# Kernel optimization log

Measured on AMD Instinct MI355X. Metric: run time of the kernel, lower is better.

Reference implementation:

```python
import jax, jax.numpy as jnp
import numpy as np
from jax import lax

RENDER_SIZE = (228, 304)   # (H, W) from __init__ default
FAR = 100.0                # z-buffer init, matches depth_map fill in source
EPS = 1e-7
CHUNK = 128                # faces processed per scan step


def setup_inputs() -> dict:
    key = jax.random.key(0)
    k1, k2, k3 = jax.random.split(key, 3)
    B, N, M = 1, 8192, 2048
    H, W = RENDER_SIZE
    uv = jax.random.uniform(k1, (B, N, 2), dtype=jnp.float32)           # u,v in [0,1]
    d = jax.random.uniform(k2, (B, N, 1), dtype=jnp.float32) * 4.0 + 1.0  # depth in [1,5]
    verts = jnp.concatenate([uv, d], axis=-1)                            # [B,N,3] depthmap format
    faces = jax.random.randint(k3, (B, M, 3), 0, N)                      # [B,M,3]
    fx = fy = 260.0
    K = jnp.array([[fx, 0.0, W / 2.0], [0.0, fy, H / 2.0], [0.0, 0.0, 1.0]], jnp.float32)
    intrinsics = jnp.tile(K[None], (B, 1, 1))
    ang = 0.02  # small camera rotation about y
    R = jnp.array([[np.cos(ang), 0.0, np.sin(ang)], [0.0, 1.0, 0.0],
                   [-np.sin(ang), 0.0, np.cos(ang)]], jnp.float32)
    R_mat = jnp.tile(R[None], (B, 1, 1))
    t_mat = jnp.tile(jnp.array([[0.01], [0.0], [0.02]], jnp.float32)[None], (B, 1, 1))
    return {"verts": verts, "faces": faces, "intrinsics": intrinsics,
            "R_mat": R_mat, "t_mat": t_mat}


def _convert_depthmap_to_cam(verts, K, H, W):
    # depthmap (u,v,d) -> camera coords; mirrors convert_depthmap_to_cam
    d = verts[..., 2:3]
    pix = jnp.concatenate([verts[..., 0:1] * W, verts[..., 1:2] * H,
                           jnp.ones_like(d)], axis=-1)                   # [B,N,3]
    Kinv = jnp.linalg.inv(K)
    return jnp.einsum('bij,bnj->bni', Kinv, pix) * d


def _project_cam_to_depthmap(cam, K, H, W):
    # camera coords -> depthmap (u,v,z); mirrors project_cam_to_depthmap
    z = cam[..., 2]
    p = jnp.stack([cam[..., 0] / (z + EPS), cam[..., 1] / (z + EPS),
                   jnp.ones_like(z)], axis=-1)
    p = jnp.einsum('bnj,bij->bni', p, K)  # matmul(p, K^T)
    u = jnp.clip(p[..., 0] / W, 0.0, 1.0)
    v = jnp.clip(p[..., 1] / H, 0.0, 1.0)
    return jnp.stack([u, v, z], axis=-1)


def _transform_depthmap(verts, K, R, t, H, W):
    cam = _convert_depthmap_to_cam(verts, K, H, W)                       # [B,N,3]
    cam2 = jnp.einsum('bij,bnj->bni', R, cam) + t[:, :, 0][:, None, :]   # R@x + t
    return _project_cam_to_depthmap(cam2, K, H, W)


def _rasterize(face_verts, S):
    """face_verts: [B,M,3,3] NDC (x,y) + depth z. Returns depth [B,S,S], sil [B,S,S]."""
    B, M = face_verts.shape[0], face_verts.shape[1]
    p = (2.0 * jnp.arange(S, dtype=face_verts.dtype) + 1.0 - S) / S      # NR pixel centers
    XP = p[None, None, None, :]   # x varies along last axis
    YP = p[None, None, :, None]   # y varies along rows

    chunks = face_verts.reshape(B, M // CHUNK, CHUNK, 3, 3).transpose(1, 0, 2, 3, 4)

    def step(carry, fvc):  # fvc: [B,C,3,3]
        depth, sil = carry
        x = fvc[..., 0][..., None, None]  # [B,C,3,1,1]
        y = fvc[..., 1][..., None, None]
        z = fvc[..., 2][..., None, None]
        x0, x1, x2 = x[:, :, 0], x[:, :, 1], x[:, :, 2]
        y0, y1, y2 = y[:, :, 0], y[:, :, 1], y[:, :, 2]
        z0, z1, z2 = z[:, :, 0], z[:, :, 1], z[:, :, 2]
        denom = (y1 - y2) * (x0 - x2) + (x2 - x1) * (y0 - y2)
        ok = jnp.abs(denom) > 1e-10
        safe = jnp.where(ok, denom, 1.0)
        w0 = ((y1 - y2) * (XP - x2) + (x2 - x1) * (YP - y2)) / safe      # [B,C,S,S]
        w1 = ((y2 - y0) * (XP - x2) + (x0 - x2) * (YP - y2)) / safe
        w2 = 1.0 - w0 - w1
        inside = (w0 >= 0) & (w1 >= 0) & (w2 >= 0) & ok
        inv_z = w0 / z0 + w1 / z1 + w2 / z2  # perspective-correct depth interp
        zp = 1.0 / jnp.where(jnp.abs(inv_z) > EPS, inv_z, EPS)
        zc = jnp.where(inside & (zp > 0), zp, FAR)
        depth = jnp.minimum(depth, zc.min(axis=1))                       # z-buffer update
        sil = jnp.maximum(sil, inside.any(axis=1).astype(depth.dtype))
        return (depth, sil), None

    init = (jnp.full((B, S, S), FAR, face_verts.dtype),
            jnp.zeros((B, S, S), face_verts.dtype))
    (depth, sil), _ = lax.scan(step, init, chunks)
    return depth, sil


def reference(verts, faces, intrinsics, R_mat, t_mat):
    H, W = RENDER_SIZE
    S = max(H, W)
    v = _transform_depthmap(verts, intrinsics, R_mat, t_mat, H, W)       # reprojected depthmap
    # depthmap [0,1] -> NDC [-1,1], keeping aspect via img_max_size
    ndc = jnp.concatenate([v[:, :, :1] * W / S * 2.0 - 1.0,
                           v[:, :, 1:2] * H / S * 2.0 - 1.0,
                           v[:, :, 2:]], axis=2)
    fv = jax.vmap(lambda vb, fb: vb[fb])(ndc, faces)                     # [B,M,3,3]
    depth, sil = _rasterize(fv, S)
    depth = depth[:, ::-1, :][:, :H, :W]  # flip(dim=1) then crop, as in _render
    sil = sil[:, ::-1, :][:, :H, :W]
    return jnp.stack([depth, sil], axis=1)  # [B,2,H,W]: depth + silhouette
```

## Files before the change

kernel.cpp:

```cpp
#include <hip/hip_runtime.h>

#define SS 304
#define HH 228
#define WW 304
#define FARV 100.0f
#define EPSV 1e-07f
#define SPLIT 16
#define CH 128

__device__ __forceinline__ void xform_vertex(
    float u, float v, float d,
    float fx, float cx, float fy, float cy,
    float r00, float r01, float r02,
    float r10, float r11, float r12,
    float r20, float r21, float r22,
    float t0, float t1, float t2,
    float& xn, float& yn, float& z)
{
#pragma clang fp contract(off)
    float ki00 = 1.0f / fx;
    float ki02 = -(cx / fx);
    float ki11 = 1.0f / fy;
    float ki12 = -(cy / fy);
    float px = u * (float)WW;
    float py = v * (float)HH;
    float c0 = (ki00 * px + ki02) * d;
    float c1 = (ki11 * py + ki12) * d;
    float c2 = d;
    float e0 = ((r00*c0 + r01*c1) + r02*c2) + t0;
    float e1 = ((r10*c0 + r11*c1) + r12*c2) + t1;
    float e2 = ((r20*c0 + r21*c1) + r22*c2) + t2;
    z = e2;
    float zd = z + EPSV;
    float p0 = e0 / zd;
    float p1 = e1 / zd;
    float q0 = p0 * fx + cx;
    float q1 = p1 * fy + cy;
    float uu = q0 / (float)WW; uu = fminf(fmaxf(uu, 0.0f), 1.0f);
    float vv = q1 / (float)HH; vv = fminf(fmaxf(vv, 0.0f), 1.0f);
    xn = uu * (float)WW / (float)SS * 2.0f - 1.0f;
    yn = vv * (float)HH / (float)SS * 2.0f - 1.0f;
}

__global__ __launch_bounds__(256) void prep_kernel(
    const float* __restrict__ verts,
    const int* __restrict__ faces,
    const float* __restrict__ Km,
    const float* __restrict__ Rm,
    const float* __restrict__ tm,
    float4* __restrict__ bboxArr,
    float4* __restrict__ G0arr,
    float4* __restrict__ G1arr,
    float2* __restrict__ G2arr,
    float* __restrict__ out, int M)
{
#pragma clang fp contract(off)
    int g = blockIdx.x * blockDim.x + threadIdx.x;
    if (g < HH * WW) {
        out[g] = FARV;
        out[HH * WW + g] = 0.0f;
    }
    if (g >= M) return;
    int m = g;
    int i0 = faces[3*m+0], i1 = faces[3*m+1], i2 = faces[3*m+2];
    float fx = Km[0], cx = Km[2], fy = Km[4], cy = Km[5];
    float r00 = Rm[0], r01 = Rm[1], r02 = Rm[2];
    float r10 = Rm[3], r11 = Rm[4], r12 = Rm[5];
    float r20 = Rm[6], r21 = Rm[7], r22 = Rm[8];
    float t0 = tm[0], t1 = tm[1], t2 = tm[2];

    float x0, y0, z0, x1, y1, z1, x2, y2, z2;
    xform_vertex(verts[3*i0+0], verts[3*i0+1], verts[3*i0+2], fx,cx,fy,cy,
                 r00,r01,r02,r10,r11,r12,r20,r21,r22,t0,t1,t2, x0,y0,z0);
    xform_vertex(verts[3*i1+0], verts[3*i1+1], verts[3*i1+2], fx,cx,fy,cy,
                 r00,r01,r02,r10,r11,r12,r20,r21,r22,t0,t1,t2, x1,y1,z1);
    xform_vertex(verts[3*i2+0], verts[3*i2+1], verts[3*i2+2], fx,cx,fy,cy,
                 r00,r01,r02,r10,r11,r12,r20,r21,r22,t0,t1,t2, x2,y2,z2);

    float A0 = y1 - y2;
    float B0 = x2 - x1;
    float A1 = y2 - y0;
    float B1 = x0 - x2;
    float dy02 = y0 - y2;
    float denom = A0 * B1 + B0 * dy02;
    bool ok = fabsf(denom) > 1e-10f;

    float xmin, xmax, ymin, ymax;
    if (ok) {
        xmin = fminf(x0, fminf(x1, x2)) - 1e-4f;
        xmax = fmaxf(x0, fmaxf(x1, x2)) + 1e-4f;
        ymin = fminf(y0, fminf(y1, y2)) - 1e-4f;
        ymax = fmaxf(y0, fmaxf(y1, y2)) + 1e-4f;
    } else {
        xmin = 1e30f; xmax = -1e30f; ymin = 1e30f; ymax = -1e30f;
    }
    bboxArr[m] = make_float4(xmin, xmax, ymin, ymax);

    float flip = (denom >= 0.0f) ? 1.0f : -1.0f;
    float sabs = fabsf(denom);
    float A0p = flip * A0, B0p = flip * B0;
    float C0p = -(A0p * x2 + B0p * y2);
    float A1p = flip * A1, B1p = flip * B1;
    float C1p = -(A1p * x2 + B1p * y2);
    float rz0 = 1.0f / z0, rz1 = 1.0f / z1, rz2 = 1.0f / z2;
    float D0 = rz0 / sabs, D1 = rz1 / sabs, D2 = rz2 / sabs;
    float d02 = D0 - D2, d12 = D1 - D2;
    float E = A0p * d02 + A1p * d12;
    float F = B0p * d02 + B1p * d12;
    float G = (C0p * d02 + C1p * d12) + sabs * D2;

    G0arr[m] = make_float4(A0p, B0p, C0p, sabs);
    G1arr[m] = make_float4(A1p, B1p, C1p, G);
    G2arr[m] = make_float2(E, F);
}

__global__ __launch_bounds__(256) void raster_kernel(
    const float4* __restrict__ bboxArr,
    const float4* __restrict__ G0arr,
    const float4* __restrict__ G1arr,
    const float2* __restrict__ G2arr,
    float* __restrict__ out, int M)
{
    __shared__ float4 sG0[CH];
    __shared__ float4 sG1[CH];
    __shared__ float2 sG2[CH];
    __shared__ int sCount;

    int tx = threadIdx.x, ty = threadIdx.y;
    int tid = ty * 16 + tx;
    int w = blockIdx.x * 16 + tx;
    int h = blockIdx.y * 16 + ty;

    int wlo = blockIdx.x * 16;
    int whi = min(wlo + 15, WW - 1);
    int hlo = blockIdx.y * 16;
    int hhi = min(hlo + 15, HH - 1);
    float txlo = ((float)(2*wlo + 1 - SS)) / (float)SS;
    float txhi = ((float)(2*whi + 1 - SS)) / (float)SS;
    float tylo = ((float)(2*(SS-1-hhi) + 1 - SS)) / (float)SS;
    float tyhi = ((float)(2*(SS-1-hlo) + 1 - SS)) / (float)SS;

    if (tid == 0) sCount = 0;
    __syncthreads();

    if (tid < CH) {
        int m = blockIdx.z * CH + tid;
        float4 rb = bboxArr[m];
        bool pass = !(rb.x > txhi || rb.y < txlo || rb.z > tyhi || rb.w < tylo);
        if (pass) {
            int i = atomicAdd(&sCount, 1);
            sG0[i] = G0arr[m];
            sG1[i] = G1arr[m];
            sG2[i] = G2arr[m];
        }
    }
    __syncthreads();
    int cnt = sCount;

    if (h < HH) {
        int irow = SS - 1 - h;
        float XP = ((float)(2*w    + 1 - SS)) / (float)SS;
        float YP = ((float)(2*irow + 1 - SS)) / (float)SS;

        float mx = 0.0f;

        for (int k = 0; k < cnt; ++k) {
            float4 g0 = sG0[k];
            float4 g1 = sG1[k];
            float2 g2 = sG2[k];
            float n0 = fmaf(g0.x, XP, fmaf(g0.y, YP, g0.z));
            float n1 = fmaf(g1.x, XP, fmaf(g1.y, YP, g1.z));
            float n2 = (g0.w - n0) - n1;
            float iz = fmaf(g2.x, XP, fmaf(g2.y, YP, g1.w));
            float m3 = fminf(fminf(n0, n1), n2);
            float cand = (m3 >= 0.0f) ? iz : 0.0f;
            mx = fmaxf(mx, cand);
        }

        if (mx > 0.0f) {
            float depth = __builtin_amdgcn_rcpf(mx);
            atomicMin((unsigned int*)&out[h * WW + w], __float_as_uint(depth));
            atomicMax((unsigned int*)&out[HH * WW + h * WW + w],
                      __float_as_uint(1.0f));
        }
    }
}

extern "C" void kernel_launch(void* const* d_in, const int* in_sizes, int n_in,
                              void* d_out, int out_size, void* d_ws, size_t ws_size,
                              hipStream_t stream) {
    const float* verts = (const float*)d_in[0];
    const int*   faces = (const int*)d_in[1];
    const float* K     = (const float*)d_in[2];
    const float* R     = (const float*)d_in[3];
    const float* t     = (const float*)d_in[4];
    float* out = (float*)d_out;

    int M = in_sizes[1] / 3;

    char* ws = (char*)d_ws;
    float4* bbox = (float4*)ws;                ws += (size_t)M * sizeof(float4);
    float4* G0   = (float4*)ws;                ws += (size_t)M * sizeof(float4);
    float4* G1   = (float4*)ws;                ws += (size_t)M * sizeof(float4);
    float2* G2   = (float2*)ws;                ws += (size_t)M * sizeof(float2);

    prep_kernel<<<(HH * WW + 255) / 256, 256, 0, stream>>>(
        verts, faces, K, R, t, bbox, G0, G1, G2, out, M);

    dim3 blk(16, 16);
    dim3 grd((WW + 15) / 16, (HH + 15) / 16, SPLIT);
    raster_kernel<<<grd, blk, 0, stream>>>(bbox, G0, G1, G2, out, M);
}
```

Measured before the change: 90.21 us.

## Rasterize 2x4 pixels per thread with incremental edge functions on 32x32 tiles

```diff
diff --git a/kernel.cpp b/kernel.cpp
--- a/kernel.cpp
+++ b/kernel.cpp
@@ -7,6 +7,7 @@
 #define EPSV 1e-07f
 #define SPLIT 16
 #define CH 128
+#define TILE 32
 
 __device__ __forceinline__ void xform_vertex(
     float u, float v, float d,
@@ -49,9 +50,9 @@
     const float* __restrict__ Rm,
     const float* __restrict__ tm,
     float4* __restrict__ bboxArr,
-    float4* __restrict__ G0arr,
-    float4* __restrict__ G1arr,
-    float2* __restrict__ G2arr,
+    float4* __restrict__ P0arr,
+    float4* __restrict__ P1arr,
+    float*  __restrict__ Garr,
     float* __restrict__ out, int M)
 {
 #pragma clang fp contract(off)
@@ -96,92 +97,117 @@
     }
     bboxArr[m] = make_float4(xmin, xmax, ymin, ymax);
 
-    float flip = (denom >= 0.0f) ? 1.0f : -1.0f;
-    float sabs = fabsf(denom);
-    float A0p = flip * A0, B0p = flip * B0;
-    float C0p = -(A0p * x2 + B0p * y2);
-    float A1p = flip * A1, B1p = flip * B1;
-    float C1p = -(A1p * x2 + B1p * y2);
+    float rs = 1.0f / denom;
+    float a0 = A0 * rs, b0 = B0 * rs;
+    float c0 = -(a0 * x2 + b0 * y2);
+    float a1 = A1 * rs, b1 = B1 * rs;
+    float c1 = -(a1 * x2 + b1 * y2);
     float rz0 = 1.0f / z0, rz1 = 1.0f / z1, rz2 = 1.0f / z2;
-    float D0 = rz0 / sabs, D1 = rz1 / sabs, D2 = rz2 / sabs;
-    float d02 = D0 - D2, d12 = D1 - D2;
-    float E = A0p * d02 + A1p * d12;
-    float F = B0p * d02 + B1p * d12;
-    float G = (C0p * d02 + C1p * d12) + sabs * D2;
-
-    G0arr[m] = make_float4(A0p, B0p, C0p, sabs);
-    G1arr[m] = make_float4(A1p, B1p, C1p, G);
-    G2arr[m] = make_float2(E, F);
-}
-
-__global__ __launch_bounds__(256) void raster_kernel(
+    float u = rz0 - rz2, v = rz1 - rz2;
+    float E = a0 * u + a1 * v;
+    float F = b0 * u + b1 * v;
+    float G = (c0 * u + c1 * v) + rz2;
+
+    P0arr[m] = make_float4(a0, b0, c0, a1);
+    P1arr[m] = make_float4(b1, c1, E, F);
+    Garr[m]  = G;
+}
+
+__global__ __launch_bounds__(128) void raster_kernel(
     const float4* __restrict__ bboxArr,
-    const float4* __restrict__ G0arr,
-    const float4* __restrict__ G1arr,
-    const float2* __restrict__ G2arr,
+    const float4* __restrict__ P0arr,
+    const float4* __restrict__ P1arr,
+    const float*  __restrict__ Garr,
     float* __restrict__ out, int M)
 {
-    __shared__ float4 sG0[CH];
-    __shared__ float4 sG1[CH];
-    __shared__ float2 sG2[CH];
+    __shared__ float4 sP0[CH];
+    __shared__ float4 sP1[CH];
+    __shared__ float  sG[CH];
     __shared__ int sCount;
 
-    int tx = threadIdx.x, ty = threadIdx.y;
+    int tx = threadIdx.x;
+    int ty = threadIdx.y;
     int tid = ty * 16 + tx;
-    int w = blockIdx.x * 16 + tx;
-    int h = blockIdx.y * 16 + ty;
-
-    int wlo = blockIdx.x * 16;
-    int whi = min(wlo + 15, WW - 1);
-    int hlo = blockIdx.y * 16;
-    int hhi = min(hlo + 15, HH - 1);
-    float txlo = ((float)(2*wlo + 1 - SS)) / (float)SS;
-    float txhi = ((float)(2*whi + 1 - SS)) / (float)SS;
-    float tylo = ((float)(2*(SS-1-hhi) + 1 - SS)) / (float)SS;
-    float tyhi = ((float)(2*(SS-1-hlo) + 1 - SS)) / (float)SS;
+
+    int wbase = blockIdx.x * TILE;
+    int hbase = blockIdx.y * TILE;
+
+    int whi = min(wbase + TILE - 1, WW - 1);
+    int hhi = min(hbase + TILE - 1, HH - 1);
+    float txlo = ((float)(2*wbase + 1 - SS)) / (float)SS;
+    float txhi = ((float)(2*whi   + 1 - SS)) / (float)SS;
+    float tylo = ((float)(2*(SS-1-hhi)   + 1 - SS)) / (float)SS;
+    float tyhi = ((float)(2*(SS-1-hbase) + 1 - SS)) / (float)SS;
 
     if (tid == 0) sCount = 0;
     __syncthreads();
 
-    if (tid < CH) {
+    {
         int m = blockIdx.z * CH + tid;
         float4 rb = bboxArr[m];
         bool pass = !(rb.x > txhi || rb.y < txlo || rb.z > tyhi || rb.w < tylo);
         if (pass) {
             int i = atomicAdd(&sCount, 1);
-            sG0[i] = G0arr[m];
-            sG1[i] = G1arr[m];
-            sG2[i] = G2arr[m];
+            sP0[i] = P0arr[m];
+            sP1[i] = P1arr[m];
+            sG[i]  = Garr[m];
         }
     }
     __syncthreads();
     int cnt = sCount;
 
-    if (h < HH) {
-        int irow = SS - 1 - h;
-        float XP = ((float)(2*w    + 1 - SS)) / (float)SS;
-        float YP = ((float)(2*irow + 1 - SS)) / (float)SS;
-
-        float mx = 0.0f;
-
-        for (int k = 0; k < cnt; ++k) {
-            float4 g0 = sG0[k];
-            float4 g1 = sG1[k];
-            float2 g2 = sG2[k];
-            float n0 = fmaf(g0.x, XP, fmaf(g0.y, YP, g0.z));
-            float n1 = fmaf(g1.x, XP, fmaf(g1.y, YP, g1.z));
-            float n2 = (g0.w - n0) - n1;
-            float iz = fmaf(g2.x, XP, fmaf(g2.y, YP, g1.w));
-            float m3 = fminf(fminf(n0, n1), n2);
-            float cand = (m3 >= 0.0f) ? iz : 0.0f;
-            mx = fmaxf(mx, cand);
+    int w0px = wbase + 2 * tx;
+    int h0px = hbase + 4 * ty;
+    float XP0 = ((float)(2*w0px + 1 - SS)) / (float)SS;
+    float YP0 = ((float)(SS - 1 - 2*h0px)) / (float)SS;
+    const float dx = 2.0f / (float)SS;
+    const float dy = -2.0f / (float)SS;
+
+    float mx[4][2] = {{0,0},{0,0},{0,0},{0,0}};
+
+    for (int k = 0; k < cnt; ++k) {
+        float4 g0 = sP0[k];
+        float4 g1 = sP1[k];
+        float  G  = sG[k];
+        float a0 = g0.x, b0 = g0.y, c0 = g0.z, a1 = g0.w;
+        float b1 = g1.x, c1 = g1.y, E = g1.z, F = g1.w;
+
+        float p0 = fmaf(a0, XP0, fmaf(b0, YP0, c0));
+        float p1 = fmaf(a1, XP0, fmaf(b1, YP0, c1));
+        float pz = fmaf(E,  XP0, fmaf(F,  YP0, G));
+        float a0dx = a0 * dx, a1dx = a1 * dx, Edx = E * dx;
+        float b0dy = b0 * dy, b1dy = b1 * dy, Fdy = F * dy;
+
+#pragma unroll
+        for (int yy = 0; yy < 4; ++yy) {
+            float w2 = (1.0f - p0) - p1;
+            float m3 = fminf(fminf(p0, p1), w2);
+            mx[yy][0] = fmaxf(mx[yy][0], (m3 >= 0.0f) ? pz : 0.0f);
+            float q0 = p0 + a0dx;
+            float q1 = p1 + a1dx;
+            float qz = pz + Edx;
+            float w2r = (1.0f - q0) - q1;
+            float m3r = fminf(fminf(q0, q1), w2r);
+            mx[yy][1] = fmaxf(mx[yy][1], (m3r >= 0.0f) ? qz : 0.0f);
+            p0 += b0dy; p1 += b1dy; pz += Fdy;
         }
-
-        if (mx > 0.0f) {
-            float depth = __builtin_amdgcn_rcpf(mx);
-            atomicMin((unsigned int*)&out[h * WW + w], __float_as_uint(depth));
-            atomicMax((unsigned int*)&out[HH * WW + h * WW + w],
-                      __float_as_uint(1.0f));
+    }
+
+#pragma unroll
+    for (int yy = 0; yy < 4; ++yy) {
+        int h = h0px + yy;
+        if (h >= HH) break;
+#pragma unroll
+        for (int xx = 0; xx < 2; ++xx) {
+            int w = w0px + xx;
+            if (w >= WW) continue;
+            float m = mx[yy][xx];
+            if (m > 0.0f) {
+                float depth = __builtin_amdgcn_rcpf(m);
+                atomicMin((unsigned int*)&out[h * WW + w], __float_as_uint(depth));
+                atomicMax((unsigned int*)&out[HH * WW + h * WW + w],
+                          __float_as_uint(1.0f));
+            }
         }
     }
 }
@@ -200,14 +226,14 @@
 
     char* ws = (char*)d_ws;
     float4* bbox = (float4*)ws;                ws += (size_t)M * sizeof(float4);
-    float4* G0   = (float4*)ws;                ws += (size_t)M * sizeof(float4);
-    float4* G1   = (float4*)ws;                ws += (size_t)M * sizeof(float4);
-    float2* G2   = (float2*)ws;                ws += (size_t)M * sizeof(float2);
+    float4* P0   = (float4*)ws;                ws += (size_t)M * sizeof(float4);
+    float4* P1   = (float4*)ws;                ws += (size_t)M * sizeof(float4);
+    float*  G    = (float*)ws;                 ws += (size_t)M * sizeof(float);
 
     prep_kernel<<<(HH * WW + 255) / 256, 256, 0, stream>>>(
-        verts, faces, K, R, t, bbox, G0, G1, G2, out, M);
-
-    dim3 blk(16, 16);
-    dim3 grd((WW + 15) / 16, (HH + 15) / 16, SPLIT);
-    raster_kernel<<<grd, blk, 0, stream>>>(bbox, G0, G1, G2, out, M);
-}
+        verts, faces, K, R, t, bbox, P0, P1, G, out, M);
+
+    dim3 blk(16, 8);
+    dim3 grd((WW + TILE - 1) / TILE, (HH + TILE - 1) / TILE, SPLIT);
+    raster_kernel<<<grd, blk, 0, stream>>>(bbox, P0, P1, G, out, M);
+}
```

New measurement: 91.88 us. About the same (+1.9%).
